# Optimization experiments

Measured on AMD Instinct MI355X. Metric: run time of the kernel, lower is better.

The kernel has to match this reference:

```python
import jax, jax.numpy as jnp
import numpy as np

N = 100000      # nodes
E = 3200000     # edges (avg degree 32)
F_IN = 512      # num_features
H = 256         # hidden
C = 64          # num_classes
K = 20          # APPNP propagation steps
ALPHA = 0.1     # teleport probability


def setup_inputs() -> dict:
    key = jax.random.key(0)
    k0, k1, k2, k3 = jax.random.split(key, 4)
    x = jax.random.normal(k0, (N, F_IN), dtype=jnp.float32)
    edge_index = jax.random.randint(k1, (2, E), 0, N, dtype=jnp.int64)
    W1 = jax.random.normal(k2, (F_IN, H), dtype=jnp.float32) / np.sqrt(F_IN).astype(np.float32)
    b1 = jnp.zeros((H,), jnp.float32)
    W2 = jax.random.normal(k3, (H, C), dtype=jnp.float32) / np.sqrt(H).astype(np.float32)
    b2 = jnpp = jnp.zeros((C,), jnp.float32)
    return {"x": x, "edge_index": edge_index, "W1": W1, "b1": b1, "W2": W2, "b2": b2}


def reference(x, edge_index, W1, b1, W2, b2):
    n = x.shape[0]
    # MLP encoder (dropout is identity in eval mode)
    h = jax.nn.relu(x @ W1 + b1) @ W2 + b2            # [N, C]

    # gcn_norm with added self-loops (PyG APPNP default)
    self_loop = jnp.arange(n, dtype=edge_index.dtype)
    src = jnp.concatenate([edge_index[0], self_loop])  # message sources
    dst = jnp.concatenate([edge_index[1], self_loop])  # aggregation targets
    deg = jax.ops.segment_sum(jnp.ones_like(dst, jnp.float32), dst, num_segments=n)
    deg_inv_sqrt = jnp.where(deg > 0, jax.lax.rsqrt(deg), 0.0)
    norm = (deg_inv_sqrt[src] * deg_inv_sqrt[dst])[:, None]  # [E+N, 1]

    def prop_step(_, z):
        msg = z[src] * norm                               # gather + scale
        agg = jax.ops.segment_sum(msg, dst, num_segments=n)  # scatter-add
        return (1.0 - ALPHA) * agg + ALPHA * h            # teleport mix

    z = jax.lax.fori_loop(0, K, prop_step, h)
    return jax.nn.log_softmax(z, axis=1)
```

## Files before the change

### kernel.cpp

```cpp
#include <hip/hip_runtime.h>
#include <hip/hip_bf16.h>
#include <math.h>

#define NN 100000
#define EE 3200000
#define FIN 512
#define HID 256
#define CLS 64
#define KST 20
#define NBUK 98
#define BCAP 36864

typedef __attribute__((ext_vector_type(8))) short bf16x8;
typedef __attribute__((ext_vector_type(4))) float f32x4;

__device__ __forceinline__ short f2bf(float f) {
    union { __hip_bfloat16 b; short s; } u;
    u.b = __float2bfloat16(f);
    return u.s;
}
__device__ __forceinline__ float bf2f(__hip_bfloat16 b) { return __bfloat162float(b); }
__device__ __forceinline__ float lobf(unsigned u) { return __uint_as_float(u << 16); }
__device__ __forceinline__ float hibf(unsigned u) { return __uint_as_float(u & 0xffff0000u); }
__device__ __forceinline__ unsigned packbf(float lo, float hi) {
    return (unsigned)(unsigned short)f2bf(lo) | ((unsigned)(unsigned short)f2bf(hi) << 16);
}


__global__ void zerocur_kernel(int* __restrict__ gcur) {
    if (threadIdx.x < NBUK) gcur[threadIdx.x] = 0;
}

__global__ __launch_bounds__(256) void bucket_kernel(const int* __restrict__ esrc,
                                                     const int* __restrict__ edst,
                                                     unsigned* __restrict__ gbuf,
                                                     int* __restrict__ gcur) {
    __shared__ int lcnt[NBUK];
    __shared__ int lbase[NBUK];
    const int t = threadIdx.x;
    for (int i = t; i < NBUK; i += 256) lcnt[i] = 0;
    __syncthreads();

    const int e0 = blockIdx.x * 2048;
    int bkt[8], rnk[8];
    unsigned rec[8];
#pragma unroll
    for (int i = 0; i < 8; ++i) {
        int idx = e0 + i * 256 + t;
        if (idx < EE) {
            int d = edst[idx];
            int s = esrc[idx];
            bkt[i] = d >> 10;
            rec[i] = ((unsigned)(d & 1023) << 17) | (unsigned)s;
            rnk[i] = atomicAdd(&lcnt[bkt[i]], 1);
        } else {
            bkt[i] = -1;
        }
    }
    __syncthreads();
    for (int i = t; i < NBUK; i += 256) lbase[i] = atomicAdd(&gcur[i], lcnt[i]);
    __syncthreads();
#pragma unroll
    for (int i = 0; i < 8; ++i)
        if (bkt[i] >= 0)
            gbuf[(size_t)bkt[i] * BCAP + lbase[bkt[i]] + rnk[i]] = rec[i];
}

__global__ void prefix_kernel(const int* __restrict__ gcur, int* __restrict__ bb,
                              int* __restrict__ rowptr) {
    if (threadIdx.x == 0) {
        int run = 0;
        for (int b = 0; b < NBUK; ++b) { bb[b] = run; run += gcur[b]; }
        bb[NBUK] = run;
        rowptr[NN] = run;
    }
}

__global__ __launch_bounds__(256) void csr_kernel(const unsigned* __restrict__ gbuf,
                                                  const int* __restrict__ gcur,
                                                  const int* __restrict__ bb,
                                                  int* __restrict__ rowptr,
                                                  float* __restrict__ dis,
                                                  int* __restrict__ csrc) {
    __shared__ int hist[1024];
    __shared__ int part[256];
    __shared__ int rp[1024];
    const int b = blockIdx.x;
    const int t = threadIdx.x;
    const int d0 = b << 10;
    const int nrec = gcur[b];
    const unsigned* rbuf = gbuf + (size_t)b * BCAP;
    const int base = bb[b];

#pragma unroll
    for (int i = 0; i < 4; ++i) hist[t * 4 + i] = 0;
    __syncthreads();
    for (int r = t; r < nrec; r += 256)
        atomicAdd(&hist[rbuf[r] >> 17], 1);
    __syncthreads();

    int h[4], sum4 = 0;
#pragma unroll
    for (int i = 0; i < 4; ++i) { h[i] = hist[t * 4 + i]; sum4 += h[i]; }
    part[t] = sum4;
    __syncthreads();
    for (int off = 1; off < 256; off <<= 1) {
        int v = (t >= off) ? part[t - off] : 0;
        __syncthreads();
        part[t] += v;
        __syncthreads();
    }

    int run = base + part[t] - sum4;
#pragma unroll
    for (int i = 0; i < 4; ++i) {
        int d = d0 + t * 4 + i;
        if (d < NN) {
            rowptr[d] = run;
            rp[t * 4 + i] = run;
            dis[d] = rsqrtf((float)(h[i] + 1));
        }
        run += h[i];
    }
#pragma unroll
    for (int i = 0; i < 4; ++i) hist[t * 4 + i] = 0;
    __syncthreads();

    for (int r = t; r < nrec; r += 256) {
        unsigned rec = rbuf[r];
        int dloc = rec >> 17;
        int pos = atomicAdd(&hist[dloc], 1);
        csrc[rp[dloc] + pos] = (int)(rec & 0x1FFFFu);
    }
}


__global__ void w1t_kernel(const float* __restrict__ W1, __hip_bfloat16* __restrict__ W1Tt) {
    const int c = threadIdx.x;
    const int kg = blockIdx.x;
    bf16x8 o;
#pragma unroll
    for (int j = 0; j < 8; ++j) o[j] = f2bf(W1[(size_t)(kg * 8 + j) * HID + c]);
    size_t dst = ((size_t)((c >> 4) * 16 + (kg >> 2))) * 512 + (c & 15) * 32 + (kg & 3) * 8;
    *(bf16x8*)((short*)W1Tt + dst) = o;
}

__global__ void w2t_kernel(const float* __restrict__ W2, __hip_bfloat16* __restrict__ W2Tt) {
    const int c = threadIdx.x;
    const int kg = blockIdx.x;
    bf16x8 o;
#pragma unroll
    for (int j = 0; j < 8; ++j) o[j] = f2bf(W2[(size_t)(kg * 8 + j) * CLS + c]);
    size_t dst = ((size_t)((c >> 4) * 8 + (kg >> 2))) * 512 + (c & 15) * 32 + (kg & 3) * 8;
    *(bf16x8*)((short*)W2Tt + dst) = o;
}


__global__ __launch_bounds__(256, 3) void mlp_kernel(const float* __restrict__ x,
                                                     const __hip_bfloat16* __restrict__ W1Tt,
                                                     const float* __restrict__ b1,
                                                     const __hip_bfloat16* __restrict__ W2Tt,
                                                     const float* __restrict__ b2,
                                                     const float* __restrict__ dis,
                                                     __hip_bfloat16* __restrict__ hb,
                                                     __hip_bfloat16* __restrict__ y0) {
    __shared__ __align__(16) char Alds[64 * 256];
    __shared__ __align__(16) char Tlds[64 * 512];

    const int t = threadIdx.x;
    const int w = t >> 6;
    const int lane = t & 63;
    const int lg = lane >> 4;
    const int li = lane & 15;
    const int loff = li * 32 + lg * 8;
    const int r0 = blockIdx.x * 64;

    const short* W1s = (const short*)W1Tt;
    const short* W2s = (const short*)W2Tt;

    const float* xp[8];
    int srow[8], sc4[8];
#pragma unroll
    for (int i = 0; i < 8; ++i) {
        int f = t + i * 256;
        srow[i] = f >> 5;
        sc4[i] = (f & 31) << 2;
        int sr = r0 + srow[i]; if (sr >= NN) sr = NN - 1;
        xp[i] = x + (size_t)sr * FIN + sc4[i];
    }

    float4 av[8];
#pragma unroll
    for (int i = 0; i < 8; ++i) av[i] = *(const float4*)(xp[i]);

    f32x4 acc1[4][4];
#pragma unroll
    for (int mf = 0; mf < 4; ++mf)
#pragma unroll
        for (int nf = 0; nf < 4; ++nf)
#pragma unroll
            for (int r = 0; r < 4; ++r) acc1[mf][nf][r] = 0.f;

    for (int kc = 0; kc < 4; ++kc) {
#pragma unroll
        for (int i = 0; i < 8; ++i) {
            short4 b;
            b.x = f2bf(av[i].x); b.y = f2bf(av[i].y); b.z = f2bf(av[i].z); b.w = f2bf(av[i].w);
            int byte = srow[i] * 256 + ((sc4[i] * 2) ^ ((srow[i] & 7) << 4));
            *(short4*)(Alds + byte) = b;
        }
        asm volatile("s_waitcnt lgkmcnt(0)" ::: "memory");
        __builtin_amdgcn_s_barrier();
        asm volatile("" ::: "memory");

        if (kc < 3) {
#pragma unroll
            for (int i = 0; i < 8; ++i) av[i] = *(const float4*)(xp[i] + (kc + 1) * 128);
        }

#pragma unroll
        for (int ks = 0; ks < 4; ++ks) {
            bf16x8 af[4], bfw[4];
#pragma unroll
            for (int mf = 0; mf < 4; ++mf) {
                int row = mf * 16 + li;
                int kb = (ks * 32 + lg * 8) * 2;
                af[mf] = *(const bf16x8*)(Alds + row * 256 + (kb ^ ((row & 7) << 4)));
            }
#pragma unroll
            for (int nf = 0; nf < 4; ++nf)
                bfw[nf] = *(const bf16x8*)(W1s + ((size_t)((w * 4 + nf) * 16 + kc * 4 + ks)) * 512 + loff);
#pragma unroll
            for (int mf = 0; mf < 4; ++mf)
#pragma unroll
                for (int nf = 0; nf < 4; ++nf)
                    acc1[mf][nf] = __builtin_amdgcn_mfma_f32_16x16x32_bf16(
                        af[mf], bfw[nf], acc1[mf][nf], 0, 0, 0);
        }
        asm volatile("" ::: "memory");
        __builtin_amdgcn_s_barrier();
        asm volatile("" ::: "memory");
    }

#pragma unroll
    for (int nf = 0; nf < 4; ++nf) {
        const float bv = b1[w * 64 + nf * 16 + li];
        const int col = w * 64 + nf * 16 + li;
#pragma unroll
        for (int mf = 0; mf < 4; ++mf) {
#pragma unroll
            for (int r = 0; r < 4; ++r) {
                int row = mf * 16 + lg * 4 + r;
                float tv = fmaxf(acc1[mf][nf][r] + bv, 0.f);
                int byte = row * 512 + ((col * 2) ^ ((row & 7) << 4));
                *(short*)(Tlds + byte) = f2bf(tv);
            }
        }
    }
    __syncthreads();

    f32x4 acc2[4];
#pragma unroll
    for (int nf = 0; nf < 4; ++nf)
#pragma unroll
        for (int r = 0; r < 4; ++r) acc2[nf][r] = 0.f;

#pragma unroll
    for (int kt2 = 0; kt2 < 8; ++kt2) {
        int row = w * 16 + li;
        int kb = (kt2 * 32 + lg * 8) * 2;
        bf16x8 at = *(const bf16x8*)(Tlds + row * 512 + (kb ^ ((row & 7) << 4)));
#pragma unroll
        for (int nf = 0; nf < 4; ++nf) {
            bf16x8 bw = *(const bf16x8*)(W2s + ((size_t)(nf * 8 + kt2)) * 512 + loff);
            acc2[nf] = __builtin_amdgcn_mfma_f32_16x16x32_bf16(at, bw, acc2[nf], 0, 0, 0);
        }
    }

#pragma unroll
    for (int r = 0; r < 4; ++r) {
        int row = r0 + w * 16 + lg * 4 + r;
        if (row < NN) {
            const float dv = dis[row];
#pragma unroll
            for (int nf = 0; nf < 4; ++nf) {
                float hv = acc2[nf][r] + b2[nf * 16 + li];
                size_t o = (size_t)row * CLS + nf * 16 + li;
                hb[o] = __float2bfloat16(hv);
                y0[o] = __float2bfloat16(hv * dv);
            }
        }
    }
}


__device__ __forceinline__ void acc8(float* a, uint4 d) {
    a[0] += lobf(d.x); a[1] += hibf(d.x);
    a[2] += lobf(d.y); a[3] += hibf(d.y);
    a[4] += lobf(d.z); a[5] += hibf(d.z);
    a[6] += lobf(d.w); a[7] += hibf(d.w);
}

template <int LAST>
__global__ __launch_bounds__(256) void prop_kernel(const __hip_bfloat16* __restrict__ yin,
                                                   const __hip_bfloat16* __restrict__ hb,
                                                   const float* __restrict__ dis,
                                                   const int* __restrict__ rowptr,
                                                   const int* __restrict__ csrc,
                                                   __hip_bfloat16* __restrict__ yout,
                                                   float* __restrict__ zout) {
    const int node = blockIdx.x * 4 + (threadIdx.x >> 6);
    const int lane = threadIdx.x & 63;
    const int g = lane >> 3;
    const int ci = lane & 7;

    const uint4* Y = (const uint4*)yin;

    int p = __builtin_amdgcn_readfirstlane(rowptr[node]);
    const int e = __builtin_amdgcn_readfirstlane(rowptr[node + 1]);

    float a[8];
#pragma unroll
    for (int j = 0; j < 8; ++j) a[j] = 0.f;

    for (; p + 32 <= e; p += 32) {
        int s0 = csrc[p + g];
        int s1 = csrc[p + 8 + g];
        int s2 = csrc[p + 16 + g];
        int s3 = csrc[p + 24 + g];
        uint4 d0 = Y[(size_t)s0 * 8 + ci];
        uint4 d1 = Y[(size_t)s1 * 8 + ci];
        uint4 d2 = Y[(size_t)s2 * 8 + ci];
        uint4 d3 = Y[(size_t)s3 * 8 + ci];
        acc8(a, d0); acc8(a, d1); acc8(a, d2); acc8(a, d3);
    }
    for (; p + 8 <= e; p += 8) {
        int s = csrc[p + g];
        uint4 d = Y[(size_t)s * 8 + ci];
        acc8(a, d);
    }
    if (p < e) {
        int q = p + g;
        int s = csrc[(q < e) ? q : (e - 1)];
        uint4 d = Y[(size_t)s * 8 + ci];
        if (q < e) acc8(a, d);
    }

#pragma unroll
    for (int j = 0; j < 8; ++j) {
        a[j] += __shfl_xor(a[j], 8);
        a[j] += __shfl_xor(a[j], 16);
        a[j] += __shfl_xor(a[j], 32);
    }

    const float din = dis[node];
    uint4 dself = Y[(size_t)node * 8 + ci];
    uint4 dh = ((const uint4*)hb)[(size_t)node * 8 + ci];
    float hv[8], z[8];
    acc8(a, dself);
    hv[0] = lobf(dh.x); hv[1] = hibf(dh.x);
    hv[2] = lobf(dh.y); hv[3] = hibf(dh.y);
    hv[4] = lobf(dh.z); hv[5] = hibf(dh.z);
    hv[6] = lobf(dh.w); hv[7] = hibf(dh.w);
#pragma unroll
    for (int j = 0; j < 8; ++j) z[j] = 0.9f * din * a[j] + 0.1f * hv[j];

    if (LAST) {
        float m = z[0];
#pragma unroll
        for (int j = 1; j < 8; ++j) m = fmaxf(m, z[j]);
        m = fmaxf(m, __shfl_xor(m, 1));
        m = fmaxf(m, __shfl_xor(m, 2));
        m = fmaxf(m, __shfl_xor(m, 4));
        float ss = 0.f;
#pragma unroll
        for (int j = 0; j < 8; ++j) ss += __expf(z[j] - m);
        ss += __shfl_xor(ss, 1);
        ss += __shfl_xor(ss, 2);
        ss += __shfl_xor(ss, 4);
        const float lgv = __logf(ss);
        if (g == 0) {
            float4 o0, o1;
            o0.x = z[0] - m - lgv; o0.y = z[1] - m - lgv; o0.z = z[2] - m - lgv; o0.w = z[3] - m - lgv;
            o1.x = z[4] - m - lgv; o1.y = z[5] - m - lgv; o1.z = z[6] - m - lgv; o1.w = z[7] - m - lgv;
            ((float4*)zout)[(size_t)node * 16 + ci * 2] = o0;
            ((float4*)zout)[(size_t)node * 16 + ci * 2 + 1] = o1;
        }
    } else {
        if (g == 0) {
            uint4 o;
            o.x = packbf(z[0] * din, z[1] * din);
            o.y = packbf(z[2] * din, z[3] * din);
            o.z = packbf(z[4] * din, z[5] * din);
            o.w = packbf(z[6] * din, z[7] * din);
            ((uint4*)yout)[(size_t)node * 8 + ci] = o;
        }
    }
}

extern "C" void kernel_launch(void* const* d_in, const int* in_sizes, int n_in,
                              void* d_out, int out_size, void* d_ws, size_t ws_size,
                              hipStream_t stream) {
    const float* x  = (const float*)d_in[0];
    const int*   ei = (const int*)d_in[1];
    const float* W1 = (const float*)d_in[2];
    const float* b1 = (const float*)d_in[3];
    const float* W2 = (const float*)d_in[4];
    const float* b2 = (const float*)d_in[5];
    float* out = (float*)d_out;

    const int* esrc = ei;
    const int* edst = ei + EE;

    char* w = (char*)d_ws;
    auto alloc = [&](size_t bytes) {
        char* p = w;
        w += (bytes + 255) & ~(size_t)255;
        return p;
    };
    __hip_bfloat16* hb   = (__hip_bfloat16*)alloc((size_t)NN * CLS * 2);
    __hip_bfloat16* yA   = (__hip_bfloat16*)alloc((size_t)NN * CLS * 2);
    __hip_bfloat16* yB   = (__hip_bfloat16*)alloc((size_t)NN * CLS * 2);
    __hip_bfloat16* W1Tt = (__hip_bfloat16*)alloc((size_t)HID * FIN * 2);
    __hip_bfloat16* W2Tt = (__hip_bfloat16*)alloc((size_t)CLS * HID * 2);
    float* dis    = (float*)alloc((size_t)NN * 4);
    int* rowptr   = (int*)alloc((size_t)(NN + 1) * 4);
    int* csrc     = (int*)alloc((size_t)EE * 4);
    unsigned* gbuf = (unsigned*)alloc((size_t)NBUK * BCAP * 4);
    int* gcur     = (int*)alloc(NBUK * 4);
    int* bb       = (int*)alloc((NBUK + 1) * 4);

    zerocur_kernel<<<1, 128, 0, stream>>>(gcur);
    bucket_kernel<<<(EE + 2047) / 2048, 256, 0, stream>>>(esrc, edst, gbuf, gcur);
    prefix_kernel<<<1, 64, 0, stream>>>(gcur, bb, rowptr);
    csr_kernel<<<NBUK, 256, 0, stream>>>(gbuf, gcur, bb, rowptr, dis, csrc);

    w1t_kernel<<<FIN / 8, HID, 0, stream>>>(W1, W1Tt);
    w2t_kernel<<<HID / 8, CLS, 0, stream>>>(W2, W2Tt);
    mlp_kernel<<<(NN + 63) / 64, 256, 0, stream>>>(x, W1Tt, b1, W2Tt, b2, dis, hb, yA);

    const __hip_bfloat16* yin = yA;
    __hip_bfloat16* yout = yB;
    for (int s = 0; s < KST - 1; ++s) {
        prop_kernel<0><<<NN / 4, 256, 0, stream>>>(yin, hb, dis, rowptr, csrc, yout, nullptr);
        const __hip_bfloat16* t2 = yin;
        yin = yout;
        yout = (__hip_bfloat16*)t2;
    }
    prop_kernel<1><<<NN / 4, 256, 0, stream>>>(yin, hb, dis, rowptr, csrc, nullptr, out);
}
```

Baseline: 1.375 ms.

## Fuse bucket prefix into CSR kernel, double-buffer MLP x loads, nontemporal prop loads

Removes the single-thread prefix kernel: each CSR block now loads the bucket counts into shared memory and computes its own base offset, and rowptr[NN] is set to the fixed edge count. The MLP encoder halves its K chunk to 64 and keeps two register buffers of x, so loads for step k+2 are issued while step k is being computed. This lowers LDS use per block. The propagation kernel uses nontemporal loads for csrc and h, which are streamed once per step, to keep the cache for gathered y rows. These changes trade one kernel launch and some x load latency for redundant per-block prefix sums and more barriers in the MLP.

```diff
diff --git a/kernel.cpp b/kernel.cpp
--- a/kernel.cpp
+++ b/kernel.cpp
@@ -13,6 +13,7 @@
 
 typedef __attribute__((ext_vector_type(8))) short bf16x8;
 typedef __attribute__((ext_vector_type(4))) float f32x4;
+typedef __attribute__((ext_vector_type(4))) unsigned u32x4;
 
 __device__ __forceinline__ short f2bf(float f) {
     union { __hip_bfloat16 b; short s; } u;
@@ -66,35 +67,29 @@
             gbuf[(size_t)bkt[i] * BCAP + lbase[bkt[i]] + rnk[i]] = rec[i];
 }
 
-__global__ void prefix_kernel(const int* __restrict__ gcur, int* __restrict__ bb,
-                              int* __restrict__ rowptr) {
-    if (threadIdx.x == 0) {
-        int run = 0;
-        for (int b = 0; b < NBUK; ++b) { bb[b] = run; run += gcur[b]; }
-        bb[NBUK] = run;
-        rowptr[NN] = run;
-    }
-}
-
 __global__ __launch_bounds__(256) void csr_kernel(const unsigned* __restrict__ gbuf,
                                                   const int* __restrict__ gcur,
-                                                  const int* __restrict__ bb,
                                                   int* __restrict__ rowptr,
                                                   float* __restrict__ dis,
                                                   int* __restrict__ csrc) {
     __shared__ int hist[1024];
     __shared__ int part[256];
     __shared__ int rp[1024];
+    __shared__ int gc[NBUK];
     const int b = blockIdx.x;
     const int t = threadIdx.x;
     const int d0 = b << 10;
-    const int nrec = gcur[b];
     const unsigned* rbuf = gbuf + (size_t)b * BCAP;
-    const int base = bb[b];
-
+
+    if (t < NBUK) gc[t] = gcur[t];
 #pragma unroll
     for (int i = 0; i < 4; ++i) hist[t * 4 + i] = 0;
     __syncthreads();
+
+    int base = 0;
+    for (int i = 0; i < b; ++i) base += gc[i];
+    const int nrec = gc[b];
+
     for (int r = t; r < nrec; r += 256)
         atomicAdd(&hist[rbuf[r] >> 17], 1);
     __syncthreads();
@@ -122,6 +117,7 @@
         }
         run += h[i];
     }
+    if (b == 0 && t == 0) rowptr[NN] = EE;
 #pragma unroll
     for (int i = 0; i < 4; ++i) hist[t * 4 + i] = 0;
     __syncthreads();
@@ -154,7 +150,6 @@
     size_t dst = ((size_t)((c >> 4) * 8 + (kg >> 2))) * 512 + (c & 15) * 32 + (kg & 3) * 8;
     *(bf16x8*)((short*)W2Tt + dst) = o;
 }
-
 
 __global__ __launch_bounds__(256, 3) void mlp_kernel(const float* __restrict__ x,
                                                      const __hip_bfloat16* __restrict__ W1Tt,
@@ -164,7 +159,7 @@
                                                      const float* __restrict__ dis,
                                                      __hip_bfloat16* __restrict__ hb,
                                                      __hip_bfloat16* __restrict__ y0) {
-    __shared__ __align__(16) char Alds[64 * 256];
+    __shared__ __align__(16) char Alds[64 * 128];
     __shared__ __align__(16) char Tlds[64 * 512];
 
     const int t = threadIdx.x;
@@ -178,20 +173,22 @@
     const short* W1s = (const short*)W1Tt;
     const short* W2s = (const short*)W2Tt;
 
-    const float* xp[8];
-    int srow[8], sc4[8];
-#pragma unroll
-    for (int i = 0; i < 8; ++i) {
+    const float* xp[4];
+    int srow[4], sc4[4];
+#pragma unroll
+    for (int i = 0; i < 4; ++i) {
         int f = t + i * 256;
-        srow[i] = f >> 5;
-        sc4[i] = (f & 31) << 2;
+        srow[i] = f >> 4;
+        sc4[i] = (f & 15) << 2;
         int sr = r0 + srow[i]; if (sr >= NN) sr = NN - 1;
         xp[i] = x + (size_t)sr * FIN + sc4[i];
     }
 
-    float4 av[8];
-#pragma unroll
-    for (int i = 0; i < 8; ++i) av[i] = *(const float4*)(xp[i]);
+    float4 av0[4], av1[4];
+#pragma unroll
+    for (int i = 0; i < 4; ++i) av0[i] = *(const float4*)(xp[i]);
+#pragma unroll
+    for (int i = 0; i < 4; ++i) av1[i] = *(const float4*)(xp[i] + 64);
 
     f32x4 acc1[4][4];
 #pragma unroll
@@ -201,46 +198,55 @@
 #pragma unroll
             for (int r = 0; r < 4; ++r) acc1[mf][nf][r] = 0.f;
 
-    for (int kc = 0; kc < 4; ++kc) {
-#pragma unroll
-        for (int i = 0; i < 8; ++i) {
-            short4 b;
-            b.x = f2bf(av[i].x); b.y = f2bf(av[i].y); b.z = f2bf(av[i].z); b.w = f2bf(av[i].w);
-            int byte = srow[i] * 256 + ((sc4[i] * 2) ^ ((srow[i] & 7) << 4));
-            *(short4*)(Alds + byte) = b;
-        }
-        asm volatile("s_waitcnt lgkmcnt(0)" ::: "memory");
-        __builtin_amdgcn_s_barrier();
-        asm volatile("" ::: "memory");
-
-        if (kc < 3) {
-#pragma unroll
-            for (int i = 0; i < 8; ++i) av[i] = *(const float4*)(xp[i] + (kc + 1) * 128);
-        }
-
-#pragma unroll
-        for (int ks = 0; ks < 4; ++ks) {
-            bf16x8 af[4], bfw[4];
-#pragma unroll
-            for (int mf = 0; mf < 4; ++mf) {
-                int row = mf * 16 + li;
-                int kb = (ks * 32 + lg * 8) * 2;
-                af[mf] = *(const bf16x8*)(Alds + row * 256 + (kb ^ ((row & 7) << 4)));
-            }
-#pragma unroll
-            for (int nf = 0; nf < 4; ++nf)
-                bfw[nf] = *(const bf16x8*)(W1s + ((size_t)((w * 4 + nf) * 16 + kc * 4 + ks)) * 512 + loff);
-#pragma unroll
-            for (int mf = 0; mf < 4; ++mf)
-#pragma unroll
-                for (int nf = 0; nf < 4; ++nf)
-                    acc1[mf][nf] = __builtin_amdgcn_mfma_f32_16x16x32_bf16(
-                        af[mf], bfw[nf], acc1[mf][nf], 0, 0, 0);
-        }
-        asm volatile("" ::: "memory");
-        __builtin_amdgcn_s_barrier();
-        asm volatile("" ::: "memory");
-    }
+#define MLP_STEP(CUR, KC)                                                            \
+    {                                                                                \
+        _Pragma("unroll")                                                            \
+        for (int i = 0; i < 4; ++i) {                                                \
+            short4 bq;                                                               \
+            bq.x = f2bf(CUR[i].x); bq.y = f2bf(CUR[i].y);                            \
+            bq.z = f2bf(CUR[i].z); bq.w = f2bf(CUR[i].w);                            \
+            int byte = srow[i] * 128 + ((sc4[i] * 2) ^ ((srow[i] & 7) << 4));        \
+            *(short4*)(Alds + byte) = bq;                                            \
+        }                                                                            \
+        asm volatile("s_waitcnt lgkmcnt(0)" ::: "memory");                           \
+        __builtin_amdgcn_s_barrier();                                                \
+        asm volatile("" ::: "memory");                                               \
+        if ((KC) + 2 < 8) {                                                          \
+            _Pragma("unroll")                                                        \
+            for (int i = 0; i < 4; ++i)                                              \
+                CUR[i] = *(const float4*)(xp[i] + ((KC) + 2) * 64);                  \
+        }                                                                            \
+        _Pragma("unroll")                                                            \
+        for (int ks = 0; ks < 2; ++ks) {                                             \
+            bf16x8 af[4], bfw[4];                                                    \
+            _Pragma("unroll")                                                        \
+            for (int mf = 0; mf < 4; ++mf) {                                         \
+                int row = mf * 16 + li;                                              \
+                int kb = ks * 64 + lg * 16;                                          \
+                af[mf] = *(const bf16x8*)(Alds + row * 128 + (kb ^ ((row & 7) << 4))); \
+            }                                                                        \
+            _Pragma("unroll")                                                        \
+            for (int nf = 0; nf < 4; ++nf)                                           \
+                bfw[nf] = *(const bf16x8*)(W1s +                                     \
+                    ((size_t)((w * 4 + nf) * 16 + (KC) * 2 + ks)) * 512 + loff);     \
+            _Pragma("unroll")                                                        \
+            for (int mf = 0; mf < 4; ++mf)                                           \
+                _Pragma("unroll")                                                    \
+                for (int nf = 0; nf < 4; ++nf)                                       \
+                    acc1[mf][nf] = __builtin_amdgcn_mfma_f32_16x16x32_bf16(          \
+                        af[mf], bfw[nf], acc1[mf][nf], 0, 0, 0);                     \
+        }                                                                            \
+        asm volatile("" ::: "memory");                                               \
+        __builtin_amdgcn_s_barrier();                                                \
+        asm volatile("" ::: "memory");                                               \
+    }
+
+#pragma unroll
+    for (int kc = 0; kc < 8; kc += 2) {
+        MLP_STEP(av0, kc);
+        MLP_STEP(av1, kc + 1);
+    }
+#undef MLP_STEP
 
 #pragma unroll
     for (int nf = 0; nf < 4; ++nf) {
@@ -294,7 +300,7 @@
 }
 
 
-__device__ __forceinline__ void acc8(float* a, uint4 d) {
+__device__ __forceinline__ void acc8(float* a, u32x4 d) {
     a[0] += lobf(d.x); a[1] += hibf(d.x);
     a[2] += lobf(d.y); a[3] += hibf(d.y);
     a[4] += lobf(d.z); a[5] += hibf(d.z);
@@ -314,7 +320,7 @@
     const int g = lane >> 3;
     const int ci = lane & 7;
 
-    const uint4* Y = (const uint4*)yin;
+    const u32x4* Y = (const u32x4*)yin;
 
     int p = __builtin_amdgcn_readfirstlane(rowptr[node]);
     const int e = __builtin_amdgcn_readfirstlane(rowptr[node + 1]);
@@ -324,25 +330,25 @@
     for (int j = 0; j < 8; ++j) a[j] = 0.f;
 
     for (; p + 32 <= e; p += 32) {
-        int s0 = csrc[p + g];
-        int s1 = csrc[p + 8 + g];
-        int s2 = csrc[p + 16 + g];
-        int s3 = csrc[p + 24 + g];
-        uint4 d0 = Y[(size_t)s0 * 8 + ci];
-        uint4 d1 = Y[(size_t)s1 * 8 + ci];
-        uint4 d2 = Y[(size_t)s2 * 8 + ci];
-        uint4 d3 = Y[(size_t)s3 * 8 + ci];
+        int s0 = __builtin_nontemporal_load(csrc + p + g);
+        int s1 = __builtin_nontemporal_load(csrc + p + 8 + g);
+        int s2 = __builtin_nontemporal_load(csrc + p + 16 + g);
+        int s3 = __builtin_nontemporal_load(csrc + p + 24 + g);
+        u32x4 d0 = Y[(size_t)s0 * 8 + ci];
+        u32x4 d1 = Y[(size_t)s1 * 8 + ci];
+        u32x4 d2 = Y[(size_t)s2 * 8 + ci];
+        u32x4 d3 = Y[(size_t)s3 * 8 + ci];
         acc8(a, d0); acc8(a, d1); acc8(a, d2); acc8(a, d3);
     }
     for (; p + 8 <= e; p += 8) {
-        int s = csrc[p + g];
-        uint4 d = Y[(size_t)s * 8 + ci];
+        int s = __builtin_nontemporal_load(csrc + p + g);
+        u32x4 d = Y[(size_t)s * 8 + ci];
         acc8(a, d);
     }
     if (p < e) {
         int q = p + g;
-        int s = csrc[(q < e) ? q : (e - 1)];
-        uint4 d = Y[(size_t)s * 8 + ci];
+        int s = __builtin_nontemporal_load(csrc + ((q < e) ? q : (e - 1)));
+        u32x4 d = Y[(size_t)s * 8 + ci];
         if (q < e) acc8(a, d);
     }
 
@@ -354,8 +360,8 @@
     }
 
     const float din = dis[node];
-    uint4 dself = Y[(size_t)node * 8 + ci];
-    uint4 dh = ((const uint4*)hb)[(size_t)node * 8 + ci];
+    u32x4 dself = Y[(size_t)node * 8 + ci];
+    u32x4 dh = __builtin_nontemporal_load((const u32x4*)hb + (size_t)node * 8 + ci);
     float hv[8], z[8];
     acc8(a, dself);
     hv[0] = lobf(dh.x); hv[1] = hibf(dh.x);
@@ -380,20 +386,20 @@
         ss += __shfl_xor(ss, 4);
         const float lgv = __logf(ss);
         if (g == 0) {
-            float4 o0, o1;
-            o0.x = z[0] - m - lgv; o0.y = z[1] - m - lgv; o0.z = z[2] - m - lgv; o0.w = z[3] - m - lgv;
-            o1.x = z[4] - m - lgv; o1.y = z[5] - m - lgv; o1.z = z[6] - m - lgv; o1.w = z[7] - m - lgv;
-            ((float4*)zout)[(size_t)node * 16 + ci * 2] = o0;
-            ((float4*)zout)[(size_t)node * 16 + ci * 2 + 1] = o1;
+            f32x4 o0, o1;
+            o0[0] = z[0] - m - lgv; o0[1] = z[1] - m - lgv; o0[2] = z[2] - m - lgv; o0[3] = z[3] - m - lgv;
+            o1[0] = z[4] - m - lgv; o1[1] = z[5] - m - lgv; o1[2] = z[6] - m - lgv; o1[3] = z[7] - m - lgv;
+            ((f32x4*)zout)[(size_t)node * 16 + ci * 2] = o0;
+            ((f32x4*)zout)[(size_t)node * 16 + ci * 2 + 1] = o1;
         }
     } else {
         if (g == 0) {
-            uint4 o;
+            u32x4 o;
             o.x = packbf(z[0] * din, z[1] * din);
             o.y = packbf(z[2] * din, z[3] * din);
             o.z = packbf(z[4] * din, z[5] * din);
             o.w = packbf(z[6] * din, z[7] * din);
-            ((uint4*)yout)[(size_t)node * 8 + ci] = o;
+            ((u32x4*)yout)[(size_t)node * 8 + ci] = o;
         }
     }
 }
@@ -428,12 +434,10 @@
     int* csrc     = (int*)alloc((size_t)EE * 4);
     unsigned* gbuf = (unsigned*)alloc((size_t)NBUK * BCAP * 4);
     int* gcur     = (int*)alloc(NBUK * 4);
-    int* bb       = (int*)alloc((NBUK + 1) * 4);
 
     zerocur_kernel<<<1, 128, 0, stream>>>(gcur);
     bucket_kernel<<<(EE + 2047) / 2048, 256, 0, stream>>>(esrc, edst, gbuf, gcur);
-    prefix_kernel<<<1, 64, 0, stream>>>(gcur, bb, rowptr);
-    csr_kernel<<<NBUK, 256, 0, stream>>>(gbuf, gcur, bb, rowptr, dis, csrc);
+    csr_kernel<<<NBUK, 256, 0, stream>>>(gbuf, gcur, rowptr, dis, csrc);
 
     w1t_kernel<<<FIN / 8, HID, 0, stream>>>(W1, W1Tt);
     w2t_kernel<<<HID / 8, CLS, 0, stream>>>(W2, W2Tt);
```

Result: slower. 1.589 ms (+15.6%).
